# Optimization experiments

Measured on AMD Instinct MI355X. Metric: run time of the kernel, lower is better.

## Reference

```python
import jax, jax.numpy as jnp
import numpy as np

EMB_DIM = 1024
NHEAD = 16
HEAD_DIM = EMB_DIM // NHEAD
SLEN = 1024
BSZ = 8
NEG_INF = -1e30


def setup_inputs() -> dict:
    key = jax.random.key(0)
    ks = jax.random.split(key, 8)
    q = jax.random.normal(ks[0], (SLEN, BSZ, EMB_DIM), dtype=jnp.float32)
    k = jax.random.normal(ks[1], (SLEN, BSZ, EMB_DIM), dtype=jnp.float32)
    v = jax.random.normal(ks[2], (SLEN, BSZ, EMB_DIM), dtype=jnp.float32)
    mask = jax.random.randint(ks[3], (BSZ * NHEAD, SLEN, SLEN), 0, 2).astype(jnp.bool_)
    # xavier_uniform bound for square [E,E] matrices
    bound = float(np.sqrt(6.0 / (EMB_DIM + EMB_DIM)))
    Wq = jax.random.uniform(ks[4], (EMB_DIM, EMB_DIM), jnp.float32, -bound, bound)
    Wk = jax.random.uniform(ks[5], (EMB_DIM, EMB_DIM), jnp.float32, -bound, bound)
    Wv = jax.random.uniform(ks[6], (EMB_DIM, EMB_DIM), jnp.float32, -bound, bound)
    Wo = jax.random.uniform(ks[7], (EMB_DIM, EMB_DIM), jnp.float32, -bound, bound)
    return {"q": q, "k": k, "v": v, "mask": mask, "Wq": Wq, "Wk": Wk, "Wv": Wv, "Wo": Wo}


def reference(q, k, v, mask, Wq, Wk, Wv, Wo):
    slen, bsz, emb = q.shape
    scaling = float(HEAD_DIM) ** -0.5
    # F.linear(x, W) = x @ W.T
    query = q @ Wq.T  # [slen, bsz, E]
    key_ = k @ Wk.T
    value = v @ Wv.T
    # -> [bsz*nhead, slen, head_dim]
    def split_heads(x):
        return x.reshape(slen, bsz * NHEAD, HEAD_DIM).transpose(1, 0, 2)
    query = split_heads(query)
    key_ = split_heads(key_)
    value = split_heads(value)
    attn_weight = jnp.einsum('bqd,bkd->bqk', query, key_) * scaling  # [B*H, S, S]
    attn_weight = jnp.where(mask, NEG_INF, attn_weight)
    attn_score = jax.nn.softmax(attn_weight, axis=-1)
    # attn_mask=True: post-softmax multiplicative mask
    attn_score = attn_score * (~mask).astype(attn_score.dtype)
    # dropout is identity in eval mode
    attn_output = jnp.einsum('bqk,bkd->bqd', attn_score, value)  # [B*H, S, hd]
    attn_output = attn_output.transpose(1, 0, 2).reshape(slen, bsz, emb)
    return attn_output @ Wo.T
```

## Files before the change

### kernel.cpp

```cpp
#include <hip/hip_runtime.h>


typedef __attribute__((ext_vector_type(8))) short bf16x8;
typedef __attribute__((ext_vector_type(8))) unsigned short u16x8;
typedef __attribute__((ext_vector_type(4))) float f32x4;

#define LOG2E 1.44269504088896340736f

__device__ __forceinline__ unsigned short bfbits(float f) {
  unsigned u = __builtin_bit_cast(unsigned, f);
  u += 0x7fffu + ((u >> 16) & 1u);
  return (unsigned short)(u >> 16);
}
__device__ __forceinline__ unsigned pk2(float a, float b) {
  return (unsigned)bfbits(a) | ((unsigned)bfbits(b) << 16);
}
__device__ __forceinline__ void async16(const void* src, void* dst_lds) {
  __builtin_amdgcn_global_load_lds(
      (const __attribute__((address_space(1))) unsigned int*)src,
      (__attribute__((address_space(3))) unsigned int*)dst_lds, 16, 0, 0);
}

__global__ void detect_mask(const unsigned* __restrict__ m, int* __restrict__ flag)
{
  unsigned ok = 1u;
#pragma unroll 8
  for (int i = 0; i < 64; ++i) {
    unsigned w = m[(threadIdx.x << 6) + i];
    ok &= (w <= 1u) ? 1u : 0u;
  }
  unsigned long long vote = __ballot(ok != 0u);
  if (threadIdx.x == 0) *flag = (vote == ~0ull) ? 1 : 0;
}

__global__ __launch_bounds__(256) void cvt_kernel(
    const float* __restrict__ q, const float* __restrict__ k, const float* __restrict__ v,
    const float* __restrict__ wq, const float* __restrict__ wk,
    const float* __restrict__ wv, const float* __restrict__ wo,
    unsigned short* __restrict__ Xin, unsigned short* __restrict__ Wbf)
{
  const unsigned u = blockIdx.x * 256u + threadIdx.x;
  const float* src;
  unsigned short* dst;
  if (u < 3145728u) {
    const unsigned z = u >> 20, r = u & 1048575u;
    src = (z == 0 ? q : z == 1 ? k : v) + (size_t)r * 8;
    dst = Xin + (size_t)z * 8388608u + (size_t)r * 8;
  } else {
    const unsigned u2 = u - 3145728u, wz = u2 >> 17, r = u2 & 131071u;
    src = (wz == 0 ? wq : wz == 1 ? wk : wz == 2 ? wv : wo) + (size_t)r * 8;
    dst = Wbf + (size_t)wz * 1048576u + (size_t)r * 8;
  }
  f32x4 a = *(const f32x4*)src;
  f32x4 b = *(const f32x4*)(src + 4);
  uint4 o;
  o.x = pk2(a[0], a[1]); o.y = pk2(a[2], a[3]);
  o.z = pk2(b[0], b[1]); o.w = pk2(b[2], b[3]);
  *(uint4*)dst = o;
}

template<int OUTF32>
__global__ __launch_bounds__(512) void gemm2ph(
    const unsigned short* __restrict__ A,
    const unsigned short* __restrict__ B,
    void* __restrict__ Cv, float scale, int M, int N, int K)
{
  const int tid = threadIdx.x;
  const int w = tid >> 6, lane = tid & 63, c = lane & 15, g = lane >> 4;
  const int wr = w >> 1, wc = w & 1;

  const int bid = blockIdx.x;
  const int swz = (bid & 7) * 32 + (bid >> 3);
  const int ntx = N >> 7;
  const int bx = swz % ntx, by = swz / ntx;
  const int rowA = by * 256, rowB = bx * 128;

  __shared__ unsigned short As[2][256 * 64];
  __shared__ unsigned short Bs[2][128 * 64];

  f32x4 acc[4][4];
#pragma unroll
  for (int i = 0; i < 4; ++i)
#pragma unroll
    for (int j = 0; j < 4; ++j) acc[i][j] = (f32x4){0.f, 0.f, 0.f, 0.f};

  const int srow = tid >> 3;
  const int skc = (tid & 7) ^ (srow & 7);
  const int wbase = (tid & ~63) * 16;

#define STAGE(kt_, bb_) do { const int k0_ = (kt_) << 6;                          \
    _Pragma("unroll") for (int i_ = 0; i_ < 4; ++i_)                              \
      async16(A + (size_t)(rowA + i_ * 64 + srow) * K + k0_ + skc * 8,            \
              (char*)&As[bb_][0] + i_ * 8192 + wbase);                            \
    _Pragma("unroll") for (int j_ = 0; j_ < 2; ++j_)                              \
      async16(B + (size_t)(rowB + j_ * 64 + srow) * K + k0_ + skc * 8,            \
              (char*)&Bs[bb_][0] + j_ * 8192 + wbase); } while (0)

#define RD(arr_, bb_, row_, ks_) \
    (*(const bf16x8*)&arr_[bb_][(row_) * 64 + ((((ks_) * 4 + g) ^ (c & 7)) << 3)])

#define COMPUTE(bb_) do {                                                         \
    bf16x8 af_[4][2], bf_[4][2];                                                  \
    _Pragma("unroll") for (int x_ = 0; x_ < 4; ++x_)                              \
      _Pragma("unroll") for (int ks_ = 0; ks_ < 2; ++ks_) {                       \
        af_[x_][ks_] = RD(As, bb_, wr * 64 + x_ * 16 + c, ks_);                   \
        bf_[x_][ks_] = RD(Bs, bb_, wc * 64 + x_ * 16 + c, ks_);                   \
      }                                                                           \
    _Pragma("unroll") for (int ks_ = 0; ks_ < 2; ++ks_)                           \
      _Pragma("unroll") for (int mf_ = 0; mf_ < 4; ++mf_)                         \
        _Pragma("unroll") for (int nf_ = 0; nf_ < 4; ++nf_)                       \
          acc[mf_][nf_] = __builtin_amdgcn_mfma_f32_16x16x32_bf16(                \
              af_[mf_][ks_], bf_[nf_][ks_], acc[mf_][nf_], 0, 0, 0); } while (0)

  STAGE(0, 0);
  STAGE(1, 1);

  for (int kt = 0; kt < 15; ++kt) {
    asm volatile("s_waitcnt vmcnt(6)" ::: "memory");
    __builtin_amdgcn_sched_barrier(0);
    __builtin_amdgcn_s_barrier();
    __builtin_amdgcn_sched_barrier(0);
    const int buf = kt & 1;
    COMPUTE(buf);
    __builtin_amdgcn_sched_barrier(0);
    __builtin_amdgcn_s_barrier();
    __builtin_amdgcn_sched_barrier(0);
    if (kt < 14) STAGE(kt + 2, buf);
  }
  asm volatile("s_waitcnt vmcnt(0)" ::: "memory");
  __builtin_amdgcn_sched_barrier(0);
  __builtin_amdgcn_s_barrier();
  __builtin_amdgcn_sched_barrier(0);
  COMPUTE(1);

#undef STAGE
#undef RD
#undef COMPUTE

  const int r0 = rowA + wr * 64, c0 = rowB + wc * 64;
  if (OUTF32) {
    float* O = (float*)Cv;
#pragma unroll
    for (int mf = 0; mf < 4; ++mf)
#pragma unroll
      for (int nf = 0; nf < 4; ++nf)
#pragma unroll
        for (int j = 0; j < 4; ++j)
          O[(size_t)(r0 + mf * 16 + g * 4 + j) * N + c0 + nf * 16 + c] = acc[mf][nf][j] * scale;
  } else {
    unsigned short* O = (unsigned short*)Cv;
#pragma unroll
    for (int mf = 0; mf < 4; ++mf)
#pragma unroll
      for (int nf = 0; nf < 4; ++nf)
#pragma unroll
        for (int j = 0; j < 4; ++j)
          O[(size_t)(r0 + mf * 16 + g * 4 + j) * N + c0 + nf * 16 + c] = bfbits(acc[mf][nf][j] * scale);
  }
}

__global__ __launch_bounds__(256) void transpose_v(
    const unsigned short* __restrict__ Xp2, unsigned short* __restrict__ Vt)
{
  const int tid = threadIdx.x;
  const int bh = blockIdx.y, b = bh >> 4, h = bh & 15;
  const int s0 = blockIdx.x << 6;
  __shared__ unsigned short T[64 * 68];
#pragma unroll
  for (int p = 0; p < 2; ++p) {
    const int idx = (p << 8) + tid, sr = idx >> 3, ch2 = idx & 7;
    *(u16x8*)&T[sr * 68 + ch2 * 8] =
        *(const u16x8*)(Xp2 + ((size_t)((s0 + sr) * 8 + b) << 10) + (h << 6) + ch2 * 8);
  }
  __syncthreads();
#pragma unroll
  for (int p = 0; p < 2; ++p) {
    const int idx = (p << 8) + tid, dr = idx >> 3, ch2 = idx & 7;
    u16x8 o;
#pragma unroll
    for (int e = 0; e < 8; ++e) o[e] = T[(ch2 * 8 + e) * 68 + dr];
    *(u16x8*)(Vt + ((size_t)(bh * 64 + dr) << 10) + s0 + ch2 * 8) = o;
  }
}

__device__ __forceinline__ void load_mask4(unsigned mv[4], const void* maskp, bool mi32,
                                           size_t base, int g) {
  if (mi32) {
    const int* mrow = (const int*)maskp + base + (g << 2);
#pragma unroll
    for (int mf = 0; mf < 4; ++mf) {
      const int4 w4 = *(const int4*)(mrow + mf * 16);
      mv[mf] = (w4.x ? 1u : 0u) | (w4.y ? 0x100u : 0u) | (w4.z ? 0x10000u : 0u) | (w4.w ? 0x1000000u : 0u);
    }
  } else {
    const unsigned char* mrow = (const unsigned char*)maskp + base + (g << 2);
#pragma unroll
    for (int mf = 0; mf < 4; ++mf) mv[mf] = *(const unsigned*)(mrow + mf * 16);
  }
}

__global__ __launch_bounds__(256) void attn_kernel(
    const unsigned short* __restrict__ Qp,
    const unsigned short* __restrict__ Kp,
    const unsigned short* __restrict__ Vt,
    const void*           __restrict__ maskp,
    const int*            __restrict__ mflag,
    unsigned short* __restrict__ AO)
{
  const int tid = threadIdx.x;
  const int w = tid >> 6, lane = tid & 63, c = lane & 15, g = lane >> 4;
  const int bh = blockIdx.y, b = bh >> 4, h = bh & 15;
  const int qb0 = blockIdx.x << 6;
  const int qrow = qb0 + (w << 4) + c;
  const bool mi32 = (*mflag != 0);

  __shared__ unsigned short Ksm[64 * 72];
  __shared__ unsigned short Vsm[64 * 72];
  __shared__ unsigned short Psm[4][16 * 72];

  bf16x8 qf[2];
  {
    const unsigned short* qp = Qp + ((size_t)(qrow * 8 + b) << 10) + (h << 6) + (g << 3);
    qf[0] = *(const bf16x8*)qp;
    qf[1] = *(const bf16x8*)(qp + 32);
  }

  const int row0 = tid >> 3, ch = tid & 7;
  const unsigned short* Vg = Vt + ((size_t)bh << 16);
  const size_t mbase0 = ((size_t)bh << 20) + ((size_t)qrow << 10);

  bf16x8 kr[2], vr[2];
#pragma unroll
  for (int p = 0; p < 2; ++p) {
    const int r = row0 + p * 32;
    kr[p] = *(const bf16x8*)(Kp + ((size_t)(r * 8 + b) << 10) + (h << 6) + (ch << 3));
    vr[p] = *(const bf16x8*)(Vg + ((size_t)r << 10) + (ch << 3));
  }
  unsigned mv[4];
  load_mask4(mv, maskp, mi32, mbase0, g);

  f32x4 oacc[4];
#pragma unroll
  for (int i = 0; i < 4; ++i) oacc[i] = (f32x4){0.f, 0.f, 0.f, 0.f};
  float mrun = -1e30f, lrun = 0.f;

  for (int t = 0; t < 16; ++t) {
    const int kk0 = t << 6;
    __syncthreads();
#pragma unroll
    for (int p = 0; p < 2; ++p) {
      const int r = row0 + p * 32;
      *(bf16x8*)&Ksm[r * 72 + (ch << 3)] = kr[p];
      *(bf16x8*)&Vsm[r * 72 + (ch << 3)] = vr[p];
    }
    __syncthreads();
    unsigned mvN[4];
    if (t < 15) {
      const int kk1 = kk0 + 64;
#pragma unroll
      for (int p = 0; p < 2; ++p) {
        const int r = row0 + p * 32;
        kr[p] = *(const bf16x8*)(Kp + ((size_t)((kk1 + r) * 8 + b) << 10) + (h << 6) + (ch << 3));
        vr[p] = *(const bf16x8*)(Vg + ((size_t)r << 10) + kk1 + (ch << 3));
      }
      load_mask4(mvN, maskp, mi32, mbase0 + kk1, g);
    }
    f32x4 sacc[4];
#pragma unroll
    for (int i = 0; i < 4; ++i) sacc[i] = (f32x4){0.f, 0.f, 0.f, 0.f};
    __builtin_amdgcn_s_setprio(1);
#pragma unroll
    for (int d2 = 0; d2 < 2; ++d2) {
#pragma unroll
      for (int mf = 0; mf < 4; ++mf) {
        bf16x8 kf = *(const bf16x8*)&Ksm[(mf * 16 + c) * 72 + d2 * 32 + (g << 3)];
        sacc[mf] = __builtin_amdgcn_mfma_f32_16x16x32_bf16(kf, qf[d2], sacc[mf], 0, 0, 0);
      }
    }
    __builtin_amdgcn_s_setprio(0);
    float tmax = -1e30f;
#pragma unroll
    for (int mf = 0; mf < 4; ++mf)
#pragma unroll
      for (int j = 0; j < 4; ++j) {
        float s = sacc[mf][j];
        if ((mv[mf] >> (8 * j)) & 0xffu) s = -1e30f;
        sacc[mf][j] = s;
        tmax = fmaxf(tmax, s);
      }
    tmax = fmaxf(tmax, __shfl_xor(tmax, 16));
    tmax = fmaxf(tmax, __shfl_xor(tmax, 32));
    const float mnew = fmaxf(mrun, tmax);
    const float alpha = __builtin_amdgcn_exp2f((mrun - mnew) * LOG2E);
    float tsum = 0.f;
    float pv[4][4];
#pragma unroll
    for (int mf = 0; mf < 4; ++mf)
#pragma unroll
      for (int j = 0; j < 4; ++j) {
        const float p = __builtin_amdgcn_exp2f((sacc[mf][j] - mnew) * LOG2E);
        pv[mf][j] = p;
        tsum += p;
      }
    tsum += __shfl_xor(tsum, 16);
    tsum += __shfl_xor(tsum, 32);
    lrun = lrun * alpha + tsum;
    mrun = mnew;
#pragma unroll
    for (int i = 0; i < 4; ++i) {
      oacc[i][0] *= alpha; oacc[i][1] *= alpha; oacc[i][2] *= alpha; oacc[i][3] *= alpha;
    }
#pragma unroll
    for (int mf = 0; mf < 4; ++mf) {
      uint2 t2;
      t2.x = pk2(pv[mf][0], pv[mf][1]);
      t2.y = pk2(pv[mf][2], pv[mf][3]);
      *(uint2*)&Psm[w][c * 72 + mf * 16 + (g << 2)] = t2;
    }
    __builtin_amdgcn_s_setprio(1);
#pragma unroll
    for (int ks = 0; ks < 2; ++ks) {
      bf16x8 pf = *(const bf16x8*)&Psm[w][c * 72 + ks * 32 + (g << 3)];
#pragma unroll
      for (int mf = 0; mf < 4; ++mf) {
        bf16x8 vf = *(const bf16x8*)&Vsm[(mf * 16 + c) * 72 + ks * 32 + (g << 3)];
        oacc[mf] = __builtin_amdgcn_mfma_f32_16x16x32_bf16(vf, pf, oacc[mf], 0, 0, 0);
      }
    }
    __builtin_amdgcn_s_setprio(0);
#pragma unroll
    for (int i = 0; i < 4; ++i) mv[i] = mvN[i];
  }
  const float inv = 1.0f / lrun;
#pragma unroll
  for (int mf = 0; mf < 4; ++mf) {
    uint2 t2;
    t2.x = pk2(oacc[mf][0] * inv, oacc[mf][1] * inv);
    t2.y = pk2(oacc[mf][2] * inv, oacc[mf][3] * inv);
    *(uint2*)(AO + ((size_t)(qrow * 8 + b) << 10) + (h << 6) + mf * 16 + (g << 2)) = t2;
  }
}

extern "C" void kernel_launch(void* const* d_in, const int* in_sizes, int n_in,
                              void* d_out, int out_size, void* d_ws, size_t ws_size,
                              hipStream_t stream)
{
  const float* q  = (const float*)d_in[0];
  const float* k  = (const float*)d_in[1];
  const float* v  = (const float*)d_in[2];
  const void*  mask = (const void*)d_in[3];
  const float* wq = (const float*)d_in[4];
  const float* wk = (const float*)d_in[5];
  const float* wv = (const float*)d_in[6];
  const float* wo = (const float*)d_in[7];

  unsigned short* ws  = (unsigned short*)d_ws;
  unsigned short* Xin = ws;
  unsigned short* Wbf = ws + 25165824u;
  unsigned short* Xp  = ws + 29360128u;
  int* mfl            = (int*)(ws + 54525952u);
  unsigned short* Vt  = ws + 8388608u;
  unsigned short* AO  = ws;

  detect_mask<<<1, 64, 0, stream>>>((const unsigned*)mask, mfl);
  cvt_kernel<<<14336, 256, 0, stream>>>(q, k, v, wq, wk, wv, wo, Xin, Wbf);
  gemm2ph<0><<<256, 512, 0, stream>>>(Xin,             Wbf,            Xp,             0.125f, 8192, 1024, 1024);
  gemm2ph<0><<<256, 512, 0, stream>>>(Xin + 8388608u,  Wbf + 1048576u, Xp + 8388608u,  1.0f,   8192, 1024, 1024);
  gemm2ph<0><<<256, 512, 0, stream>>>(Xin + 16777216u, Wbf + 2097152u, Xp + 16777216u, 1.0f,   8192, 1024, 1024);
  transpose_v<<<dim3(16, 128), 256, 0, stream>>>(Xp + 16777216u, Vt);
  attn_kernel<<<dim3(16, 128), 256, 0, stream>>>(Xp, Xp + 8388608u, Vt, mask, mfl, AO);
  gemm2ph<1><<<256, 512, 0, stream>>>(AO, Wbf + 3145728u, d_out, 1.0f, 8192, 1024, 1024);
}
```

Baseline: 309.4 us.

## Batch QKV projections into one launch with 128x128 tiles and smaller blocks

Replaces the 256x128-tile, 512-thread GEMM with a 128x128-tile, 256-thread variant. The three Q/K/V projection GEMMs now run as a single 1536-block launch, with the block index selecting the projection. The smaller tiles give more blocks and better CU coverage on the many-CU device, and merging the launches removes inter-kernel gaps, at the cost of less operand reuse per tile. The attention kernel also drops its s_setprio priority bumps around the MFMA sections.

```diff
diff --git a/kernel.cpp b/kernel.cpp
--- a/kernel.cpp
+++ b/kernel.cpp
@@ -60,22 +60,27 @@
 }
 
 template<int OUTF32>
-__global__ __launch_bounds__(512) void gemm2ph(
-    const unsigned short* __restrict__ A,
-    const unsigned short* __restrict__ B,
-    void* __restrict__ Cv, float scale, int M, int N, int K)
+__global__ __launch_bounds__(256) void gemm128(
+    const unsigned short* __restrict__ A0,
+    const unsigned short* __restrict__ B0,
+    void* __restrict__ C0, float scale0, int M, int N, int K)
 {
   const int tid = threadIdx.x;
   const int w = tid >> 6, lane = tid & 63, c = lane & 15, g = lane >> 4;
   const int wr = w >> 1, wc = w & 1;
 
   const int bid = blockIdx.x;
-  const int swz = (bid & 7) * 32 + (bid >> 3);
+  const int p = bid >> 9, local = bid & 511;
+  const unsigned short* A = A0 + (size_t)p * 8388608u;
+  const unsigned short* B = B0 + (size_t)p * 1048576u;
+  const float scale = (p == 0) ? scale0 : 1.0f;
+
+  const int swz = (local & 7) * 64 + (local >> 3);
   const int ntx = N >> 7;
   const int bx = swz % ntx, by = swz / ntx;
-  const int rowA = by * 256, rowB = bx * 128;
-
-  __shared__ unsigned short As[2][256 * 64];
+  const int rowA = by * 128, rowB = bx * 128;
+
+  __shared__ unsigned short As[2][128 * 64];
   __shared__ unsigned short Bs[2][128 * 64];
 
   f32x4 acc[4][4];
@@ -84,20 +89,21 @@
 #pragma unroll
     for (int j = 0; j < 4; ++j) acc[i][j] = (f32x4){0.f, 0.f, 0.f, 0.f};
 
-  const int srow = tid >> 3;
-  const int skc = (tid & 7) ^ (srow & 7);
   const int wbase = (tid & ~63) * 16;
 
 #define STAGE(kt_, bb_) do { const int k0_ = (kt_) << 6;                          \
-    _Pragma("unroll") for (int i_ = 0; i_ < 4; ++i_)                              \
-      async16(A + (size_t)(rowA + i_ * 64 + srow) * K + k0_ + skc * 8,            \
-              (char*)&As[bb_][0] + i_ * 8192 + wbase);                            \
-    _Pragma("unroll") for (int j_ = 0; j_ < 2; ++j_)                              \
-      async16(B + (size_t)(rowB + j_ * 64 + srow) * K + k0_ + skc * 8,            \
-              (char*)&Bs[bb_][0] + j_ * 8192 + wbase); } while (0)
+    _Pragma("unroll") for (int i_ = 0; i_ < 4; ++i_) {                            \
+      const int slot_ = i_ * 256 + tid;                                           \
+      const int row_ = slot_ >> 3;                                                \
+      const int kc_ = (slot_ & 7) ^ (row_ & 7);                                   \
+      async16(A + (size_t)(rowA + row_) * K + k0_ + kc_ * 8,                      \
+              (char*)&As[bb_][0] + (i_ << 12) + wbase);                           \
+      async16(B + (size_t)(rowB + row_) * K + k0_ + kc_ * 8,                      \
+              (char*)&Bs[bb_][0] + (i_ << 12) + wbase);                           \
+    } } while (0)
 
 #define RD(arr_, bb_, row_, ks_) \
-    (*(const bf16x8*)&arr_[bb_][(row_) * 64 + ((((ks_) * 4 + g) ^ (c & 7)) << 3)])
+    (*(const bf16x8*)&arr_[bb_][(row_) * 64 + ((((ks_) * 4 + g) ^ ((row_) & 7)) << 3)])
 
 #define COMPUTE(bb_) do {                                                         \
     bf16x8 af_[4][2], bf_[4][2];                                                  \
@@ -116,7 +122,7 @@
   STAGE(1, 1);
 
   for (int kt = 0; kt < 15; ++kt) {
-    asm volatile("s_waitcnt vmcnt(6)" ::: "memory");
+    asm volatile("s_waitcnt vmcnt(8)" ::: "memory");
     __builtin_amdgcn_sched_barrier(0);
     __builtin_amdgcn_s_barrier();
     __builtin_amdgcn_sched_barrier(0);
@@ -139,7 +145,7 @@
 
   const int r0 = rowA + wr * 64, c0 = rowB + wc * 64;
   if (OUTF32) {
-    float* O = (float*)Cv;
+    float* O = (float*)C0;
 #pragma unroll
     for (int mf = 0; mf < 4; ++mf)
 #pragma unroll
@@ -148,7 +154,7 @@
         for (int j = 0; j < 4; ++j)
           O[(size_t)(r0 + mf * 16 + g * 4 + j) * N + c0 + nf * 16 + c] = acc[mf][nf][j] * scale;
   } else {
-    unsigned short* O = (unsigned short*)Cv;
+    unsigned short* O = (unsigned short*)C0 + (size_t)p * 8388608u;
 #pragma unroll
     for (int mf = 0; mf < 4; ++mf)
 #pragma unroll
@@ -268,7 +274,6 @@
     f32x4 sacc[4];
 #pragma unroll
     for (int i = 0; i < 4; ++i) sacc[i] = (f32x4){0.f, 0.f, 0.f, 0.f};
-    __builtin_amdgcn_s_setprio(1);
 #pragma unroll
     for (int d2 = 0; d2 < 2; ++d2) {
 #pragma unroll
@@ -277,7 +282,6 @@
         sacc[mf] = __builtin_amdgcn_mfma_f32_16x16x32_bf16(kf, qf[d2], sacc[mf], 0, 0, 0);
       }
     }
-    __builtin_amdgcn_s_setprio(0);
     float tmax = -1e30f;
 #pragma unroll
     for (int mf = 0; mf < 4; ++mf)
@@ -317,7 +321,6 @@
       t2.y = pk2(pv[mf][2], pv[mf][3]);
       *(uint2*)&Psm[w][c * 72 + mf * 16 + (g << 2)] = t2;
     }
-    __builtin_amdgcn_s_setprio(1);
 #pragma unroll
     for (int ks = 0; ks < 2; ++ks) {
       bf16x8 pf = *(const bf16x8*)&Psm[w][c * 72 + ks * 32 + (g << 3)];
@@ -327,7 +330,6 @@
         oacc[mf] = __builtin_amdgcn_mfma_f32_16x16x32_bf16(vf, pf, oacc[mf], 0, 0, 0);
       }
     }
-    __builtin_amdgcn_s_setprio(0);
 #pragma unroll
     for (int i = 0; i < 4; ++i) mv[i] = mvN[i];
   }
@@ -364,10 +366,8 @@
 
   detect_mask<<<1, 64, 0, stream>>>((const unsigned*)mask, mfl);
   cvt_kernel<<<14336, 256, 0, stream>>>(q, k, v, wq, wk, wv, wo, Xin, Wbf);
-  gemm2ph<0><<<256, 512, 0, stream>>>(Xin,             Wbf,            Xp,             0.125f, 8192, 1024, 1024);
-  gemm2ph<0><<<256, 512, 0, stream>>>(Xin + 8388608u,  Wbf + 1048576u, Xp + 8388608u,  1.0f,   8192, 1024, 1024);
-  gemm2ph<0><<<256, 512, 0, stream>>>(Xin + 16777216u, Wbf + 2097152u, Xp + 16777216u, 1.0f,   8192, 1024, 1024);
+  gemm128<0><<<1536, 256, 0, stream>>>(Xin, Wbf, Xp, 0.125f, 8192, 1024, 1024);
   transpose_v<<<dim3(16, 128), 256, 0, stream>>>(Xp + 16777216u, Vt);
   attn_kernel<<<dim3(16, 128), 256, 0, stream>>>(Xp, Xp + 8388608u, Vt, mask, mfl, AO);
-  gemm2ph<1><<<256, 512, 0, stream>>>(AO, Wbf + 3145728u, d_out, 1.0f, 8192, 1024, 1024);
-}
+  gemm128<1><<<512, 256, 0, stream>>>(AO, Wbf + 3145728u, d_out, 1.0f, 8192, 1024, 1024);
+}
```

Result: faster. 292.3 us (-5.5%).
